# Optimization experiments

Measured on AMD Instinct MI355X. Metric: run time of the kernel, lower is better.

## Reference

```python
import jax, jax.numpy as jnp
import numpy as np

BITS = 4
N_PACK = 8  # 32-bit container / 4-bit values
GROUPSIZE = 128
MASK = (1 << BITS) - 1


def _unpack(packed, n_valid):
    # packed: [R, ceil(n_valid/N_PACK)] int32 -> [R, n_valid] int32 nibbles
    shifts = (jnp.arange(N_PACK, dtype=jnp.int32) * BITS)
    vals = (packed[:, :, None] >> shifts) & MASK  # [R, C, N_PACK]
    return vals.reshape(packed.shape[0], -1)[:, :n_valid]


def setup_inputs() -> dict:
    key = jax.random.key(0)
    k0, k1, k2, k3, k4 = jax.random.split(key, 5)
    O, I = 4096, 4096
    ng = I // GROUPSIZE  # 32
    x = jax.random.normal(k0, (2, 2048, I), dtype=jnp.float32)
    packed_weight = jax.random.randint(k1, (O, I // N_PACK), 0, 2147483647, dtype=jnp.int32)
    scale = jax.random.uniform(k2, (O, ng), dtype=jnp.float32)
    packed_zp = jax.random.randint(k3, (O, (ng + N_PACK - 1) // N_PACK), 0, 2147483647, dtype=jnp.int32)
    bias = jax.random.normal(k4, (O,), dtype=jnp.float32)
    return {"x": x, "packed_weight": packed_weight, "scale": scale,
            "packed_zp": packed_zp, "bias": bias}


def reference(x, packed_weight, scale, packed_zp, bias):
    O, ng = scale.shape
    I = packed_weight.shape[1] * N_PACK
    # unpack uint4 weights and zero-points (matches torch recover(): shift+mask)
    w_int = _unpack(packed_weight, I)          # [O, I] values in [0, 15]
    zp_int = _unpack(packed_zp, ng)            # [O, ng]
    # per-group dequant: (w - zp) * scale
    w = w_int.reshape(O, ng, GROUPSIZE).astype(scale.dtype)
    fp_weight = ((w - zp_int[:, :, None].astype(scale.dtype)) * scale[:, :, None]).reshape(O, I)
    # F.linear: x @ W^T + b
    return jnp.einsum('bsi,oi->bso', x, fp_weight) + bias
```

## Files before the change

kernel.cpp:

```cpp
#include <hip/hip_runtime.h>
#include <stdint.h>

typedef __attribute__((ext_vector_type(4))) float  floatx4;
typedef __attribute__((ext_vector_type(8))) short  shortx8;
typedef __attribute__((ext_vector_type(4))) unsigned short ushortx4;

typedef unsigned int   u32;
typedef unsigned short u16;

#define TILE    128
#define BK      64
#define THREADS 256
#define CHUNK   (TILE * BK)

__device__ __forceinline__ u32 pack2bf(float f0, float f1) {
    u32 u0 = __builtin_bit_cast(u32, f0) + 0x8000u;
    u32 u1 = __builtin_bit_cast(u32, f1) + 0x8000u;
    return __builtin_amdgcn_perm(u1, u0, 0x07060302u);
}

__device__ __forceinline__ unsigned short f2bf(float f) {
    u32 u = __builtin_bit_cast(u32, f);
    u += 0x7FFFu + ((u >> 16) & 1u);
    return (unsigned short)(u >> 16);
}

__global__ __launch_bounds__(THREADS)
void prep_kernel(const float* __restrict__ x, const int* __restrict__ pw,
                 const float* __restrict__ scale, const int* __restrict__ pzp,
                 u16* __restrict__ At, u16* __restrict__ Bt,
                 int M, int O, int I, int ng, int lsSeg, int lsG) {
    const int NT = gridDim.x * THREADS;
    const int t0 = blockIdx.x * THREADS + threadIdx.x;
    const int segsPerRow = I >> 3;

    const int Sx = (M * I) >> 3;
    for (int s = t0; s < Sx; s += NT) {
        const float4 v0 = ((const float4*)x)[(size_t)s * 2];
        const float4 v1 = ((const float4*)x)[(size_t)s * 2 + 1];
        u32 p[4];
        p[0] = pack2bf(v0.x, v0.y); p[1] = pack2bf(v0.z, v0.w);
        p[2] = pack2bf(v1.x, v1.y); p[3] = pack2bf(v1.z, v1.w);
        ((uint4*)At)[s] = *(uint4*)p;
    }

    const int Sw = (O * I) >> 3;
    for (int s = t0; s < Sw; s += NT) {
        const u32 wq = (u32)pw[s];
        const int o    = s >> lsSeg;
        const int wcol = s & (segsPerRow - 1);
        const int g    = wcol >> lsG;
        const float sc = scale[o * ng + g];
        const int zpw  = pzp[o * ((ng + 7) >> 3) + (g >> 3)];
        const int zp   = (zpw >> ((g & 7) * 4)) & 15;
        const float nzc = -sc * (float)(zp + 128);
        float v[8];
        #pragma unroll
        for (int j = 0; j < 8; j++) {
            u32 tt;
            if (j < 4)       tt = (wq << (16 - 4 * j)) & 0x000F0000u;
            else if (j == 4) tt = wq & 0x000F0000u;
            else             tt = (wq >> (4 * j - 16)) & 0x000F0000u;
            v[j] = __builtin_fmaf(__builtin_bit_cast(float, tt | 0x43000000u), sc, nzc);
        }
        u32 p[4];
        p[0] = pack2bf(v[0], v[1]); p[1] = pack2bf(v[2], v[3]);
        p[2] = pack2bf(v[4], v[5]); p[3] = pack2bf(v[6], v[7]);
        ((uint4*)Bt)[s] = *(uint4*)p;
    }
}

#define VM8 asm volatile("s_waitcnt vmcnt(8)" ::: "memory")
#define VM4 asm volatile("s_waitcnt vmcnt(4)" ::: "memory")
#define VM0 asm volatile("s_waitcnt vmcnt(0)" ::: "memory")

#define GTILE(T, DOISS, WAITSTMT) do {                                                    \
    const u16* __restrict__ sb = &S[((T) & 3) * 16384];                                   \
    u16* nb = &S[(((T) + 3) & 3) * 16384];                                                \
    shortx8 af[4], bfr[4];                                                                \
    _Pragma("unroll")                                                                     \
    for (int i = 0; i < 4; i++) af[i]  = *(const shortx8*)(sb + rdA + i * 1024);          \
    _Pragma("unroll")                                                                     \
    for (int j = 0; j < 4; j++) bfr[j] = *(const shortx8*)(sb + rdB + j * 1024);          \
    if (DOISS) {                                                                          \
        _Pragma("unroll")                                                                 \
        for (int l = 0; l < 2; l++)                                                       \
            __builtin_amdgcn_global_load_lds((const __attribute__((address_space(1))) u32*)(g[l]), \
                (__attribute__((address_space(3))) u32*)(nb + ldsoff[l]), 16, 0, 0);      \
    }                                                                                     \
    __builtin_amdgcn_s_barrier();                                                         \
    __builtin_amdgcn_s_setprio(1);                                                        \
    _Pragma("unroll")                                                                     \
    for (int i = 0; i < 4; i++)                                                           \
        _Pragma("unroll")                                                                 \
        for (int j = 0; j < 4; j++)                                                       \
            acc[i][j] = __builtin_amdgcn_mfma_f32_16x16x32_bf16(af[i], bfr[j], acc[i][j], 0, 0, 0); \
    __builtin_amdgcn_s_setprio(0);                                                        \
    __builtin_amdgcn_s_barrier();                                                         \
    _Pragma("unroll")                                                                     \
    for (int i = 0; i < 4; i++) af[i] = *(const shortx8*)(sb + rdA + 4096 + i * 1024);    \
    if (DOISS) {                                                                          \
        _Pragma("unroll")                                                                 \
        for (int l = 2; l < 4; l++)                                                       \
            __builtin_amdgcn_global_load_lds((const __attribute__((address_space(1))) u32*)(g[l]), \
                (__attribute__((address_space(3))) u32*)(nb + ldsoff[l]), 16, 0, 0);      \
        _Pragma("unroll")                                                                 \
        for (int l = 0; l < 4; l++) g[l] += 32;                                           \
    }                                                                                     \
    __builtin_amdgcn_s_barrier();                                                         \
    __builtin_amdgcn_s_setprio(1);                                                        \
    _Pragma("unroll")                                                                     \
    for (int i = 0; i < 4; i++)                                                           \
        _Pragma("unroll")                                                                 \
        for (int j = 0; j < 4; j++)                                                       \
            acc[i + 4][j] = __builtin_amdgcn_mfma_f32_16x16x32_bf16(af[i], bfr[j], acc[i + 4][j], 0, 0, 0); \
    __builtin_amdgcn_s_setprio(0);                                                        \
    WAITSTMT;                                                                             \
    __builtin_amdgcn_s_barrier();                                                         \
} while (0)

__global__ __launch_bounds__(512, 2)
void gemm256(const u16* __restrict__ At, const u16* __restrict__ Bt,
             const float* __restrict__ bias, float* __restrict__ out,
             int O, int I, int KT) {
    __shared__ u16 S[4 * 16384];

    const int tid = threadIdx.x;
    const int nblk_n = O / 256;

    int bid = blockIdx.x;
    const int nwg = gridDim.x;
    if ((nwg & 7) == 0) {
        const int q = nwg >> 3;
        bid = (bid & 7) * q + (bid >> 3);
    }
    const int mt = bid / nblk_n, nt = bid % nblk_n;

    const int w = tid >> 6, lane = tid & 63;
    const int wm = w >> 2, wn = w & 3;
    const int l15 = lane & 15, l4 = lane >> 4;
    const int sw  = l15 & 7;

    const int rdA = (wm * 128 + l15) * 64 + ((l4 ^ sw) * 8);
    const int rdB = (wn * 64  + l15) * 64 + ((((l4 | 4) ^ sw)) * 8);

    const u16* g[4];
    int ldsoff[4];
    #pragma unroll
    for (int l = 0; l < 4; l++) {
        const int s   = (w * 4 + l) * 64 + lane;
        const int row = s >> 3;
        const int k   = (s & 7) ^ (row & 7);
        ldsoff[l] = (w * 4 + l) * 512 + lane * 8;
        g[l] = (k < 4) ? (At + (size_t)(mt * 256 + row) * I + k * 8)
                       : (Bt + (size_t)(nt * 256 + row) * I + (k - 4) * 8);
    }

    floatx4 acc[8][4];
    #pragma unroll
    for (int i = 0; i < 8; i++)
        #pragma unroll
        for (int j = 0; j < 4; j++)
            acc[i][j] = (floatx4){0.f, 0.f, 0.f, 0.f};

    #pragma unroll
    for (int p = 0; p < 3; p++) {
        u16* sb = &S[p * 16384];
        #pragma unroll
        for (int l = 0; l < 4; l++)
            __builtin_amdgcn_global_load_lds((const __attribute__((address_space(1))) u32*)(g[l]),
                (__attribute__((address_space(3))) u32*)(sb + ldsoff[l]), 16, 0, 0);
        #pragma unroll
        for (int l = 0; l < 4; l++) g[l] += 32;
    }
    VM8;
    __builtin_amdgcn_s_barrier();

    int t = 0;
    for (; t < KT - 3; ++t) GTILE(t, 1, VM8);
    GTILE(t, 0, VM4); ++t;
    GTILE(t, 0, VM0); ++t;
    GTILE(t, 0, (void)0);

    #pragma unroll
    for (int j = 0; j < 4; j++) {
        int col  = nt * 256 + wn * 64 + j * 16 + l15;
        float bv = bias[col];
        #pragma unroll
        for (int i = 0; i < 8; i++) {
            int rowb = mt * 256 + wm * 128 + i * 16 + l4 * 4;
            #pragma unroll
            for (int r = 0; r < 4; r++)
                out[(size_t)(rowb + r) * O + col] = acc[i][j][r] + bv;
        }
    }
}

__global__ __launch_bounds__(THREADS, 2)
void gemm_bf16(const u16* __restrict__ At, const u16* __restrict__ Bt,
               const float* __restrict__ bias, float* __restrict__ out,
               int O, int I, int KT) {
    __shared__ u16 As[CHUNK];
    __shared__ u16 Bs[CHUNK];

    const int tid = threadIdx.x;
    const int nblk_n = O / TILE;
    const int mt = blockIdx.x / nblk_n;
    const int nt = blockIdx.x % nblk_n;
    const int w = tid >> 6, lane = tid & 63;
    const int wm = w >> 1, wn = w & 1;
    const int l15 = lane & 15, l4 = lane >> 4;
    const int sw  = l15 & 7;

    const int sr = tid >> 3;
    const int sc = (tid & 7) ^ (sr & 7);

    floatx4 acc[4][4];
    #pragma unroll
    for (int i = 0; i < 4; i++)
        #pragma unroll
        for (int j = 0; j < 4; j++)
            acc[i][j] = (floatx4){0.f, 0.f, 0.f, 0.f};

    const u16* gaBase = At + ((size_t)(mt * TILE) + sr) * I + sc * 8;
    const u16* gbBase = Bt + ((size_t)(nt * TILE) + sr) * I + sc * 8;

    for (int kt = 0; kt < KT; kt++) {
        const u16* ga = gaBase + kt * BK;
        const u16* gb = gbBase + kt * BK;
        __syncthreads();
        #pragma unroll
        for (int it = 0; it < 4; it++) {
            const int ldsOff = it * 2048 + tid * 8;
            const size_t gOff = (size_t)(it * 32) * I;
            __builtin_amdgcn_global_load_lds((const __attribute__((address_space(1))) u32*)(ga + gOff),
                                             (__attribute__((address_space(3))) u32*)(As + ldsOff),
                                             16, 0, 0);
            __builtin_amdgcn_global_load_lds((const __attribute__((address_space(1))) u32*)(gb + gOff),
                                             (__attribute__((address_space(3))) u32*)(Bs + ldsOff),
                                             16, 0, 0);
        }
        __syncthreads();

        #pragma unroll
        for (int ks = 0; ks < 2; ks++) {
            shortx8 af[4], bfr[4];
            #pragma unroll
            for (int i = 0; i < 4; i++)
                af[i] = *(const shortx8*)(&As[(wm * 64 + i * 16 + l15) * BK + ((ks * 4 + l4) ^ sw) * 8]);
            #pragma unroll
            for (int j = 0; j < 4; j++)
                bfr[j] = *(const shortx8*)(&Bs[(wn * 64 + j * 16 + l15) * BK + ((ks * 4 + l4) ^ sw) * 8]);
            #pragma unroll
            for (int i = 0; i < 4; i++)
                #pragma unroll
                for (int j = 0; j < 4; j++)
                    acc[i][j] = __builtin_amdgcn_mfma_f32_16x16x32_bf16(af[i], bfr[j], acc[i][j], 0, 0, 0);
        }
    }

    #pragma unroll
    for (int j = 0; j < 4; j++) {
        int col  = nt * TILE + wn * 64 + j * 16 + l15;
        float bv = bias[col];
        #pragma unroll
        for (int i = 0; i < 4; i++) {
            int rowb = mt * TILE + wm * 64 + i * 16 + l4 * 4;
            #pragma unroll
            for (int r = 0; r < 4; r++)
                out[(size_t)(rowb + r) * O + col] = acc[i][j][r] + bv;
        }
    }
}

#define LDA 72
__global__ __launch_bounds__(THREADS, 2)
void wql_fused(const float* __restrict__ x, const int* __restrict__ pw,
               const float* __restrict__ scale, const int* __restrict__ pzp,
               const float* __restrict__ bias, float* __restrict__ out,
               int M, int O, int I, int ng)
{
    __shared__ unsigned short As[TILE * LDA];
    __shared__ unsigned short Bs[TILE * LDA];
    const int tid = threadIdx.x;
    const int nblk_n = O / TILE;
    const int mt = blockIdx.x / nblk_n, nt = blockIdx.x % nblk_n;
    const int w = tid >> 6, lane = tid & 63;
    const int wm = w >> 1, wn = w & 1;
    const int l15 = lane & 15, l4 = lane >> 4;
    const int pw_rowlen = I / 8, zp_rowlen = (ng + 7) / 8, GS = I / ng;

    floatx4 acc[4][4];
    #pragma unroll
    for (int i = 0; i < 4; i++)
        #pragma unroll
        for (int j = 0; j < 4; j++) acc[i][j] = (floatx4){0.f, 0.f, 0.f, 0.f};

    const int nk = I / BK;
    for (int kt = 0; kt < nk; kt++) {
        __syncthreads();
        #pragma unroll
        for (int it = 0; it < 8; it++) {
            int f = tid + it * THREADS;
            int row = f >> 4, seg = f & 15;
            const float4 v = *(const float4*)(x + (size_t)(mt * TILE + row) * I + kt * BK + seg * 4);
            ushortx4 b;
            b.x = f2bf(v.x); b.y = f2bf(v.y); b.z = f2bf(v.z); b.w = f2bf(v.w);
            *(ushortx4*)(&As[row * LDA + seg * 4]) = b;
        }
        const int g = (kt * BK) / GS;
        #pragma unroll
        for (int it = 0; it < 4; it++) {
            int e = tid + it * THREADS;
            int row = e >> 3, c = e & 7;
            int o = nt * TILE + row;
            int wq = pw[(size_t)o * pw_rowlen + kt * (BK / 8) + c];
            float s = scale[o * ng + g];
            int zpw = pzp[o * zp_rowlen + (g >> 3)];
            int zp = (zpw >> ((g & 7) * 4)) & 15;
            shortx8 b;
            #pragma unroll
            for (int j = 0; j < 8; j++) {
                int nib = (wq >> (4 * j)) & 15;
                b[j] = (short)f2bf((float)(nib - zp) * s);
            }
            *(shortx8*)(&Bs[row * LDA + c * 8]) = b;
        }
        __syncthreads();
        #pragma unroll
        for (int ks = 0; ks < 2; ks++) {
            shortx8 af[4], bfr[4];
            #pragma unroll
            for (int i = 0; i < 4; i++)
                af[i] = *(const shortx8*)(&As[(wm * 64 + i * 16 + l15) * LDA + ks * 32 + l4 * 8]);
            #pragma unroll
            for (int j = 0; j < 4; j++)
                bfr[j] = *(const shortx8*)(&Bs[(wn * 64 + j * 16 + l15) * LDA + ks * 32 + l4 * 8]);
            #pragma unroll
            for (int i = 0; i < 4; i++)
                #pragma unroll
                for (int j = 0; j < 4; j++)
                    acc[i][j] = __builtin_amdgcn_mfma_f32_16x16x32_bf16(af[i], bfr[j], acc[i][j], 0, 0, 0);
        }
    }
    #pragma unroll
    for (int j = 0; j < 4; j++) {
        int col = nt * TILE + wn * 64 + j * 16 + l15;
        float bv = bias[col];
        #pragma unroll
        for (int i = 0; i < 4; i++) {
            int rowb = mt * TILE + wm * 64 + i * 16 + l4 * 4;
            #pragma unroll
            for (int r = 0; r < 4; r++)
                out[(size_t)(rowb + r) * O + col] = acc[i][j][r] + bv;
        }
    }
}

extern "C" void kernel_launch(void* const* d_in, const int* in_sizes, int n_in,
                              void* d_out, int out_size, void* d_ws, size_t ws_size,
                              hipStream_t stream) {
    const float* x     = (const float*)d_in[0];
    const int*   pw    = (const int*)d_in[1];
    const float* scale = (const float*)d_in[2];
    const int*   pzp   = (const int*)d_in[3];
    const float* bias  = (const float*)d_in[4];
    float*       out   = (float*)d_out;

    const int O  = in_sizes[4];
    const int ng = in_sizes[2] / O;
    const int I  = (in_sizes[1] / O) * 8;
    const int M  = in_sizes[0] / I;
    int lsSeg = 0; { int v = I >> 3; while ((1 << lsSeg) < v) lsSeg++; }
    int lsG = 0;   { int v = (I / ng) >> 3; while ((1 << lsG) < v) lsG++; }

    const size_t need = ((size_t)M * I + (size_t)O * I) * sizeof(u16);
    if (ws_size >= need) {
        u16* At = (u16*)d_ws;
        u16* Bt = At + (size_t)M * I;
        prep_kernel<<<dim3(2048), THREADS, 0, stream>>>(x, pw, scale, pzp, At, Bt, M, O, I, ng, lsSeg, lsG);
        const bool ok256 = (M % 256 == 0) && (O % 256 == 0) && (I % 32 == 0) && (I / 32 >= 8);
        if (ok256) {
            gemm256<<<dim3((M / 256) * (O / 256)), 512, 0, stream>>>(At, Bt, bias, out, O, I, I / 32);
        } else {
            gemm_bf16<<<dim3((M / TILE) * (O / TILE)), THREADS, 0, stream>>>(At, Bt, bias, out, O, I, I / BK);
        }
    } else {
        wql_fused<<<dim3((M / TILE) * (O / TILE)), THREADS, 0, stream>>>(x, pw, scale, pzp, bias, out, M, O, I, ng);
    }
}
```

Measured before the change: 257.1 us.

## Software-pipeline LDS fragment reads with MFMA using double-buffered register fragments

Restructures the main loop of the 256-tile GEMM so each half-step loads the next set of A/B fragments from LDS while MFMAs run on the previously loaded fragments held in double-buffered registers. This removes one barrier per k-tile and overlaps LDS reads with matrix math. The loop is unrolled by 4 over the LDS ring buffers, and the launch guard now requires the k-tile count to be a multiple of 4. Register pressure grows with the extra fragment buffers, which may hurt occupancy at two blocks per CU, and the waits now also drain lgkmcnt.

```diff
diff --git a/kernel.cpp b/kernel.cpp
--- a/kernel.cpp
+++ b/kernel.cpp
@@ -70,53 +70,56 @@
     }
 }
 
-#define VM8 asm volatile("s_waitcnt vmcnt(8)" ::: "memory")
-#define VM4 asm volatile("s_waitcnt vmcnt(4)" ::: "memory")
-#define VM0 asm volatile("s_waitcnt vmcnt(0)" ::: "memory")
-
-#define GTILE(T, DOISS, WAITSTMT) do {                                                    \
-    const u16* __restrict__ sb = &S[((T) & 3) * 16384];                                   \
-    u16* nb = &S[(((T) + 3) & 3) * 16384];                                                \
-    shortx8 af[4], bfr[4];                                                                \
-    _Pragma("unroll")                                                                     \
-    for (int i = 0; i < 4; i++) af[i]  = *(const shortx8*)(sb + rdA + i * 1024);          \
-    _Pragma("unroll")                                                                     \
-    for (int j = 0; j < 4; j++) bfr[j] = *(const shortx8*)(sb + rdB + j * 1024);          \
-    if (DOISS) {                                                                          \
-        _Pragma("unroll")                                                                 \
-        for (int l = 0; l < 2; l++)                                                       \
-            __builtin_amdgcn_global_load_lds((const __attribute__((address_space(1))) u32*)(g[l]), \
-                (__attribute__((address_space(3))) u32*)(nb + ldsoff[l]), 16, 0, 0);      \
-    }                                                                                     \
-    __builtin_amdgcn_s_barrier();                                                         \
-    __builtin_amdgcn_s_setprio(1);                                                        \
-    _Pragma("unroll")                                                                     \
-    for (int i = 0; i < 4; i++)                                                           \
-        _Pragma("unroll")                                                                 \
-        for (int j = 0; j < 4; j++)                                                       \
-            acc[i][j] = __builtin_amdgcn_mfma_f32_16x16x32_bf16(af[i], bfr[j], acc[i][j], 0, 0, 0); \
-    __builtin_amdgcn_s_setprio(0);                                                        \
-    __builtin_amdgcn_s_barrier();                                                         \
-    _Pragma("unroll")                                                                     \
-    for (int i = 0; i < 4; i++) af[i] = *(const shortx8*)(sb + rdA + 4096 + i * 1024);    \
-    if (DOISS) {                                                                          \
-        _Pragma("unroll")                                                                 \
-        for (int l = 2; l < 4; l++)                                                       \
-            __builtin_amdgcn_global_load_lds((const __attribute__((address_space(1))) u32*)(g[l]), \
-                (__attribute__((address_space(3))) u32*)(nb + ldsoff[l]), 16, 0, 0);      \
-        _Pragma("unroll")                                                                 \
-        for (int l = 0; l < 4; l++) g[l] += 32;                                           \
-    }                                                                                     \
-    __builtin_amdgcn_s_barrier();                                                         \
-    __builtin_amdgcn_s_setprio(1);                                                        \
-    _Pragma("unroll")                                                                     \
-    for (int i = 0; i < 4; i++)                                                           \
-        _Pragma("unroll")                                                                 \
-        for (int j = 0; j < 4; j++)                                                       \
-            acc[i + 4][j] = __builtin_amdgcn_mfma_f32_16x16x32_bf16(af[i], bfr[j], acc[i + 4][j], 0, 0, 0); \
-    __builtin_amdgcn_s_setprio(0);                                                        \
-    WAITSTMT;                                                                             \
-    __builtin_amdgcn_s_barrier();                                                         \
+
+#define VM8L asm volatile("s_waitcnt vmcnt(8) lgkmcnt(0)" ::: "memory")
+#define VM4L asm volatile("s_waitcnt vmcnt(4) lgkmcnt(0)" ::: "memory")
+#define VM0L asm volatile("s_waitcnt vmcnt(0) lgkmcnt(0)" ::: "memory")
+
+#define ISSUE(GP, NB, LO)                                                                  \
+    __builtin_amdgcn_global_load_lds((const __attribute__((address_space(1))) u32*)(GP),   \
+        (__attribute__((address_space(3))) u32*)((NB) + (LO)), 16, 0, 0)
+
+#define R1(BUFC, BUFN, P, DOISS, DOMFMA) do {                                              \
+    const u16* __restrict__ sb = S + (BUFC) * 16384;                                       \
+    u16* nb = S + (BUFN) * 16384;                                                          \
+    _Pragma("unroll")                                                                      \
+    for (int i = 0; i < 4; i++) aflo[P][i] = *(const shortx8*)(sb + rdA + i * 1024);       \
+    _Pragma("unroll")                                                                      \
+    for (int j = 0; j < 4; j++) bfr[P][j]  = *(const shortx8*)(sb + rdB + j * 1024);       \
+    if (DOISS) { ISSUE(g[0], nb, ldsoff[0]); ISSUE(g[1], nb, ldsoff[1]); }                 \
+    if (DOMFMA) {                                                                          \
+        __builtin_amdgcn_s_setprio(1);                                                     \
+        _Pragma("unroll")                                                                  \
+        for (int i = 0; i < 4; i++)                                                        \
+            _Pragma("unroll")                                                              \
+            for (int j = 0; j < 4; j++)                                                    \
+                acc[i + 4][j] = __builtin_amdgcn_mfma_f32_16x16x32_bf16(                   \
+                    afhi[(P) ^ 1][i], bfr[(P) ^ 1][j], acc[i + 4][j], 0, 0, 0);            \
+        __builtin_amdgcn_s_setprio(0);                                                     \
+    }                                                                                      \
+    __builtin_amdgcn_s_barrier();                                                          \
+} while (0)
+
+#define R2(BUFC, BUFN, P, DOISS, WAITS) do {                                               \
+    const u16* __restrict__ sb = S + (BUFC) * 16384;                                       \
+    u16* nb = S + (BUFN) * 16384;                                                          \
+    _Pragma("unroll")                                                                      \
+    for (int i = 0; i < 4; i++) afhi[P][i] = *(const shortx8*)(sb + rdA + 4096 + i * 1024);\
+    if (DOISS) {                                                                           \
+        ISSUE(g[2], nb, ldsoff[2]); ISSUE(g[3], nb, ldsoff[3]);                            \
+        _Pragma("unroll")                                                                  \
+        for (int l = 0; l < 4; l++) g[l] += 32;                                            \
+    }                                                                                      \
+    __builtin_amdgcn_s_setprio(1);                                                         \
+    _Pragma("unroll")                                                                      \
+    for (int i = 0; i < 4; i++)                                                            \
+        _Pragma("unroll")                                                                  \
+        for (int j = 0; j < 4; j++)                                                        \
+            acc[i][j] = __builtin_amdgcn_mfma_f32_16x16x32_bf16(                           \
+                aflo[P][i], bfr[P][j], acc[i][j], 0, 0, 0);                                \
+    __builtin_amdgcn_s_setprio(0);                                                         \
+    WAITS;                                                                                 \
+    __builtin_amdgcn_s_barrier();                                                          \
 } while (0)
 
 __global__ __launch_bounds__(512, 2)
@@ -163,24 +166,43 @@
         for (int j = 0; j < 4; j++)
             acc[i][j] = (floatx4){0.f, 0.f, 0.f, 0.f};
 
+    shortx8 aflo[2][4], afhi[2][4], bfr[2][4];
+
     #pragma unroll
     for (int p = 0; p < 3; p++) {
         u16* sb = &S[p * 16384];
         #pragma unroll
         for (int l = 0; l < 4; l++)
-            __builtin_amdgcn_global_load_lds((const __attribute__((address_space(1))) u32*)(g[l]),
-                (__attribute__((address_space(3))) u32*)(sb + ldsoff[l]), 16, 0, 0);
+            ISSUE(g[l], sb, ldsoff[l]);
         #pragma unroll
         for (int l = 0; l < 4; l++) g[l] += 32;
     }
-    VM8;
+    asm volatile("s_waitcnt vmcnt(8)" ::: "memory");
     __builtin_amdgcn_s_barrier();
 
-    int t = 0;
-    for (; t < KT - 3; ++t) GTILE(t, 1, VM8);
-    GTILE(t, 0, VM4); ++t;
-    GTILE(t, 0, VM0); ++t;
-    GTILE(t, 0, (void)0);
+    R1(0, 3, 0, 1, 0);
+    R2(0, 3, 0, 1, VM8L);
+
+    const int iters = (KT - 4) >> 2;
+    for (int it = 0; it < iters; ++it) {
+        R1(1, 0, 1, 1, 1); R2(1, 0, 1, 1, VM8L);
+        R1(2, 1, 0, 1, 1); R2(2, 1, 0, 1, VM8L);
+        R1(3, 2, 1, 1, 1); R2(3, 2, 1, 1, VM8L);
+        R1(0, 3, 0, 1, 1); R2(0, 3, 0, 1, VM8L);
+    }
+
+    R1(1, 0, 1, 0, 1); R2(1, 0, 1, 0, VM4L);
+    R1(2, 1, 0, 0, 1); R2(2, 1, 0, 0, VM0L);
+    R1(3, 2, 1, 0, 1); R2(3, 2, 1, 0, (void)0);
+
+    __builtin_amdgcn_s_setprio(1);
+    #pragma unroll
+    for (int i = 0; i < 4; i++)
+        #pragma unroll
+        for (int j = 0; j < 4; j++)
+            acc[i + 4][j] = __builtin_amdgcn_mfma_f32_16x16x32_bf16(
+                afhi[1][i], bfr[1][j], acc[i + 4][j], 0, 0, 0);
+    __builtin_amdgcn_s_setprio(0);
 
     #pragma unroll
     for (int j = 0; j < 4; j++) {
@@ -244,18 +266,18 @@
 
         #pragma unroll
         for (int ks = 0; ks < 2; ks++) {
-            shortx8 af[4], bfr[4];
+            shortx8 af[4], bfr2[4];
             #pragma unroll
             for (int i = 0; i < 4; i++)
                 af[i] = *(const shortx8*)(&As[(wm * 64 + i * 16 + l15) * BK + ((ks * 4 + l4) ^ sw) * 8]);
             #pragma unroll
             for (int j = 0; j < 4; j++)
-                bfr[j] = *(const shortx8*)(&Bs[(wn * 64 + j * 16 + l15) * BK + ((ks * 4 + l4) ^ sw) * 8]);
+                bfr2[j] = *(const shortx8*)(&Bs[(wn * 64 + j * 16 + l15) * BK + ((ks * 4 + l4) ^ sw) * 8]);
             #pragma unroll
             for (int i = 0; i < 4; i++)
                 #pragma unroll
                 for (int j = 0; j < 4; j++)
-                    acc[i][j] = __builtin_amdgcn_mfma_f32_16x16x32_bf16(af[i], bfr[j], acc[i][j], 0, 0, 0);
+                    acc[i][j] = __builtin_amdgcn_mfma_f32_16x16x32_bf16(af[i], bfr2[j], acc[i][j], 0, 0, 0);
         }
     }
 
@@ -329,18 +351,18 @@
         __syncthreads();
         #pragma unroll
         for (int ks = 0; ks < 2; ks++) {
-            shortx8 af[4], bfr[4];
+            shortx8 af[4], bfr2[4];
             #pragma unroll
             for (int i = 0; i < 4; i++)
                 af[i] = *(const shortx8*)(&As[(wm * 64 + i * 16 + l15) * LDA + ks * 32 + l4 * 8]);
             #pragma unroll
             for (int j = 0; j < 4; j++)
-                bfr[j] = *(const shortx8*)(&Bs[(wn * 64 + j * 16 + l15) * LDA + ks * 32 + l4 * 8]);
+                bfr2[j] = *(const shortx8*)(&Bs[(wn * 64 + j * 16 + l15) * LDA + ks * 32 + l4 * 8]);
             #pragma unroll
             for (int i = 0; i < 4; i++)
                 #pragma unroll
                 for (int j = 0; j < 4; j++)
-                    acc[i][j] = __builtin_amdgcn_mfma_f32_16x16x32_bf16(af[i], bfr[j], acc[i][j], 0, 0, 0);
+                    acc[i][j] = __builtin_amdgcn_mfma_f32_16x16x32_bf16(af[i], bfr2[j], acc[i][j], 0, 0, 0);
         }
     }
     #pragma unroll
@@ -379,9 +401,10 @@
         u16* At = (u16*)d_ws;
         u16* Bt = At + (size_t)M * I;
         prep_kernel<<<dim3(2048), THREADS, 0, stream>>>(x, pw, scale, pzp, At, Bt, M, O, I, ng, lsSeg, lsG);
-        const bool ok256 = (M % 256 == 0) && (O % 256 == 0) && (I % 32 == 0) && (I / 32 >= 8);
+        const int KT32 = I / 32;
+        const bool ok256 = (M % 256 == 0) && (O % 256 == 0) && (I % 128 == 0) && (KT32 >= 8) && ((KT32 & 3) == 0);
         if (ok256) {
-            gemm256<<<dim3((M / 256) * (O / 256)), 512, 0, stream>>>(At, Bt, bias, out, O, I, I / 32);
+            gemm256<<<dim3((M / 256) * (O / 256)), 512, 0, stream>>>(At, Bt, bias, out, O, I, KT32);
         } else {
             gemm_bf16<<<dim3((M / TILE) * (O / TILE)), THREADS, 0, stream>>>(At, Bt, bias, out, O, I, I / BK);
         }
```

Measured after the change: 243.8 us. -5.2%, faster.
